# Optimization experiments

Measured on AMD Instinct MI355X. Metric: run time of the kernel, lower is better.

Reference implementation:

```python
import jax, jax.numpy as jnp
import numpy as np

N = 20000   # nodes
E = 320000  # edges
T = 12      # sequence_length
H = 64      # hidden_dim
CIN = 16    # input_dim_per_step
L = 3       # num_st_layers
BN_EPS = 1e-5


def setup_inputs() -> dict:
    key = jax.random.key(0)
    ks = jax.random.split(key, 30)
    s = 0.05
    rn = lambda k, shp: jax.random.normal(k, shp, jnp.float32) * s
    inp = {
        "x": jax.random.normal(ks[0], (N, T * CIN), jnp.float32),
        "edge_index": jax.random.randint(ks[1], (2, E), 0, N, jnp.int32),
        # embedding
        "We": rn(ks[2], (CIN, H)), "be": rn(ks[3], (H,)),
        # stacked per-layer params for the 3 ST layers
        "gcn_W": rn(ks[4], (L, H, H)), "gcn_b": rn(ks[5], (L, H)),
        "conv_w": rn(ks[6], (L, H, H, 3)), "conv_b": rn(ks[7], (L, H)),
        "bn_g": jnp.ones((L, H), jnp.float32), "bn_b": rn(ks[8], (L, H)),
        "bn_m": rn(ks[9], (L, H)),
        "bn_v": jax.random.uniform(ks[10], (L, H), jnp.float32, 0.5, 1.5),
        # temporal attention MLP (H -> H//2 -> 1)
        "ta_w1": rn(ks[11], (H, H // 2)), "ta_b1": rn(ks[12], (H // 2,)),
        "ta_w2": rn(ks[13], (H // 2, 1)), "ta_b2": rn(ks[14], (1,)),
        # feature attention MLP (T -> T//2 -> 1)
        "fa_w1": rn(ks[15], (T, T // 2)), "fa_b1": rn(ks[16], (T // 2,)),
        "fa_w2": rn(ks[17], (T // 2, 1)), "fa_b2": rn(ks[18], (1,)),
        # output MLP (H -> H//2 -> 1)
        "ow1": rn(ks[19], (H, H // 2)), "ob1": rn(ks[20], (H // 2,)),
        "ow2": rn(ks[21], (H // 2, 1)), "ob2": rn(ks[22], (1,)),
    }
    return inp


def reference(x, edge_index, We, be, gcn_W, gcn_b, conv_w, conv_b,
              bn_g, bn_b, bn_m, bn_v, ta_w1, ta_b1, ta_w2, ta_b2,
              fa_w1, fa_b1, fa_w2, fa_b2, ow1, ob1, ow2, ob2):
    n = x.shape[0]
    # --- GCN normalization with self-loops (PyG gcn_norm) ---
    loops = jnp.arange(n, dtype=edge_index.dtype)
    src = jnp.concatenate([edge_index[0], loops])
    dst = jnp.concatenate([edge_index[1], loops])
    deg = jax.ops.segment_sum(jnp.ones_like(src, jnp.float32), dst, num_segments=n)
    dinv = 1.0 / jnp.sqrt(deg)  # deg >= 1 thanks to self-loops
    coef = dinv[src] * dinv[dst]  # [E+N]

    # --- per-timestep embedding (vectorized over t) ---
    xr = x.reshape(n, T, CIN)
    emb = jax.nn.relu(jnp.einsum('ntc,ch->nth', xr, We) + be)  # [N,T,H]
    x_st = emb.reshape(n, T * H)

    # --- ST layers (replicating original row-major .view layout mixing) ---
    for i in range(L):
        xi = x_st.reshape(n, H, T)  # [N,C,T]
        # GCNConv per timestep, batched over t: linear then normalized aggregate
        h = jnp.einsum('nct,cd->ndt', xi, gcn_W[i])          # [N,H,T]
        msg = coef[:, None, None] * h[src]                   # [E+N,H,T]
        agg = jax.ops.segment_sum(msg, dst, num_segments=n) + gcn_b[i][None, :, None]
        # temporal conv (kernel 3, pad 1) over T
        tmp = jax.lax.conv_general_dilated(
            agg, conv_w[i], (1,), [(1, 1)],
            dimension_numbers=('NCH', 'OIH', 'NCH')) + conv_b[i][None, :, None]
        # BatchNorm1d (eval mode: running stats)
        normed = (tmp - bn_m[i][None, :, None]) / jnp.sqrt(bn_v[i][None, :, None] + BN_EPS)
        normed = normed * bn_g[i][None, :, None] + bn_b[i][None, :, None]
        # residual is Identity (in_channels == out_channels)
        x_st = jax.nn.relu(normed + xi).reshape(n, H * T)

    # --- dual attention pooling ---
    xa = x_st.reshape(n, T, H)
    tw = (jnp.einsum('ntm,mk->ntk', jax.nn.relu(jnp.einsum('nth,hm->ntm', xa, ta_w1) + ta_b1), ta_w2) + ta_b2)[..., 0]
    tw = jax.nn.softmax(tw, axis=1)                          # [N,T]
    xt = (xa * tw[..., None]).transpose(0, 2, 1)             # [N,H,T]
    fw = (jnp.einsum('nhm,mk->nhk', jax.nn.relu(jnp.einsum('nht,tm->nhm', xt, fa_w1) + fa_b1), fa_w2) + fa_b2)[..., 0]
    fw = jax.nn.softmax(fw, axis=1)                          # [N,H]
    x_final = jnp.sum(xt * fw[..., None], axis=2)            # [N,H]

    # --- output MLP (dropout is identity in eval) ---
    out = jax.nn.relu(x_final @ ow1 + ob1) @ ow2 + ob2       # [N,1]
    return out
```

## Files before the change

kernel.cpp:

```cpp
#include <hip/hip_runtime.h>
#include <cstddef>
#include <cstdint>

#define T_ 12
#define H_ 64
#define CIN_ 16
#define F_ 768
#define BN_EPS 1e-5f
#define ECAP 80
#define RPITCH 88
#define SLOTS 64

typedef float v2f __attribute__((ext_vector_type(2)));
typedef short s8v __attribute__((ext_vector_type(8)));
typedef float f4v __attribute__((ext_vector_type(4)));

__device__ __forceinline__ unsigned short f2bf(float f) {
    unsigned u = __float_as_uint(f);
    unsigned r = (u + 0x7FFFu + ((u >> 16) & 1u)) >> 16;
    return (unsigned short)r;
}
__device__ __forceinline__ float bf2f(unsigned short h) {
    return __uint_as_float(((unsigned)h) << 16);
}
__device__ __forceinline__ v2f bf2x2(unsigned u) {
    v2f r;
    r.x = __uint_as_float(u << 16);
    r.y = __uint_as_float(u & 0xFFFF0000u);
    return r;
}
__device__ __forceinline__ v2f pkfma(v2f a, v2f b, v2f c) {
    return __builtin_elementwise_fma(a, b, c);
}


__global__ void k_init(int* __restrict__ cursor, int n) {
    int i = blockIdx.x * 256 + threadIdx.x;
    if (i < n) cursor[i] = 0;
}


__global__ __launch_bounds__(256) void k_fused(
        const float* __restrict__ gcn_W, const float* __restrict__ gcn_b,
        const float* __restrict__ conv_w,
        float* __restrict__ wkp, float* __restrict__ bkp,
        const int* __restrict__ srcv, const int* __restrict__ dstv,
        int* __restrict__ cursor, int* __restrict__ csr_src, int e,
        const float* __restrict__ x, const float* __restrict__ We,
        const float* __restrict__ be, unsigned short* __restrict__ xbf, int nT,
        int nbE) {
    __shared__ float sW[CIN_ * H_];
    __shared__ float sb[H_];
    int b = blockIdx.x;
    int tid = threadIdx.x;

    if (b < 36) {
        int l = b / 12, k = (b / 4) % 3, cq = b & 3;
        const float* Wg = gcn_W + (size_t)l * 4096;
        const float* cw = conv_w + (size_t)l * 12288;
#pragma unroll
        for (int j = 0; j < 4; j++) {
            int idx = j * 256 + tid;
            int c = cq * 16 + (idx >> 6);
            int o = idx & 63;
            float acc = 0.f;
            for (int d = 0; d < 64; d++)
                acc += Wg[c * 64 + d] * cw[(size_t)(o * 64 + d) * 3 + k];
            wkp[(((size_t)l * 3 + k) * 64 + c) * 64 + o] = acc;
        }
        if (cq == 0 && tid < 64) {
            int o = tid;
            const float* gb = gcn_b + (size_t)l * 64;
            float acc = 0.f;
            for (int d = 0; d < 64; d++)
                acc += gb[d] * cw[(size_t)(o * 64 + d) * 3 + k];
            bkp[((size_t)l * 3 + k) * 64 + o] = acc;
        }
        return;
    }
    if (b < 36 + nbE) {
        int i = (b - 36) * 256 + tid;
        if (i < e) {
            int d = dstv[i], s = srcv[i];
            int pos = atomicAdd(&cursor[d], 1);
            if (pos < SLOTS) csr_src[d * SLOTS + pos] = s;
        }
        return;
    }
    for (int i = tid; i < CIN_ * H_; i += 256) sW[i] = We[i];
    if (tid < H_) sb[tid] = be[tid];
    __syncthreads();
    int h4  = tid & 15;
    int ntl = tid >> 4;
    int nt  = (b - 36 - nbE) * 16 + ntl;
    if (nt >= nT) return;
    const float4* xp = (const float4*)(x + (size_t)nt * CIN_);
    float4 xv4[4];
    xv4[0] = xp[0]; xv4[1] = xp[1]; xv4[2] = xp[2]; xv4[3] = xp[3];
    const float* xs = (const float*)xv4;
    float acc[4];
#pragma unroll
    for (int j = 0; j < 4; j++) acc[j] = sb[h4 * 4 + j];
#pragma unroll
    for (int c = 0; c < CIN_; c++) {
        float4 w = *(const float4*)&sW[c * H_ + h4 * 4];
        float xc = xs[c];
        acc[0] += xc * w.x; acc[1] += xc * w.y;
        acc[2] += xc * w.z; acc[3] += xc * w.w;
    }
    ushort4 h;
    h.x = f2bf(fmaxf(acc[0], 0.f)); h.y = f2bf(fmaxf(acc[1], 0.f));
    h.z = f2bf(fmaxf(acc[2], 0.f)); h.w = f2bf(fmaxf(acc[3], 0.f));
    *(ushort4*)&xbf[(size_t)nt * H_ + h4 * 4] = h;
}


__global__ __launch_bounds__(256) void k_post(
        const float* __restrict__ wkp, unsigned short* __restrict__ wkA,
        const int* __restrict__ cursor, const int* __restrict__ csr_src,
        float* __restrict__ csr_coef, float* __restrict__ dinv, int n) {
    int b = blockIdx.x;
    int tid = threadIdx.x;
    if (b < 18) {
        int wave = tid >> 6, lane = tid & 63;
        int job = b * 4 + wave;
        int l = job / 24, rem = job % 24;
        int mt = rem / 6, ks = rem % 6;
        int o = mt * 16 + (lane & 15);
        int kbase = ks * 32 + (lane >> 4) * 8;
#pragma unroll
        for (int j = 0; j < 8; j++) {
            int k = kbase + j;
            int kk = k >> 6, c = k & 63;
            float v = wkp[(((size_t)l * 3 + kk) * 64 + c) * 64 + o];
            wkA[((((size_t)l * 24) + mt * 6 + ks) * 64 + lane) * 8 + j] = f2bf(v);
        }
        return;
    }
    int i = (b - 18) * 256 + tid;
    int node = i >> 6, slot = i & 63;
    if (node >= n) return;
    int deg = cursor[node];
    float dn = rsqrtf((float)(deg + 1));
    if (slot == 0) dinv[node] = dn;
    if (slot < min(deg, SLOTS)) {
        int s = csr_src[node * SLOTS + slot];
        csr_coef[node * SLOTS + slot] = rsqrtf((float)(cursor[s] + 1)) * dn;
    }
}


#define BPK(aL, aH, c2, u) { \
    aL = pkfma(bf2x2((u).x), c2, aL); \
    aH = pkfma(bf2x2((u).y), c2, aH); }

#define LAYER_GATHER_CONV()                                                    \
    int tid = threadIdx.x;                                                     \
    int n0 = blockIdx.x * 8;                                                   \
    int wave = tid >> 6, lane = tid & 63;                                      \
    int wbase = wave * (ECAP * 2);                                             \
    for (int i = tid; i < 8 * 2 * RPITCH; i += 256) {                          \
        int s = i / (2 * RPITCH);                                              \
        int r = i - s * (2 * RPITCH);                                          \
        int row = (r < RPITCH) ? 0 : 13;                                       \
        int c = (r < RPITCH) ? r : r - RPITCH;                                 \
        sxb[s * 14 * RPITCH + row * RPITCH + c] = 0;                           \
    }                                                                          \
    int begs[2], cnts[2], stgs[2], epos[2];                                    \
    {                                                                          \
        int pos = 0;                                                           \
        for (int si = 0; si < 2; si++) {                                       \
            int nn = n0 + wave * 2 + si; if (nn >= n) nn = n - 1;              \
            int beg = nn * SLOTS;                                              \
            int cnt = min(degv[nn], SLOTS);                                    \
            int stg = min(cnt, ECAP - pos);                                    \
            for (int i = lane; i < stg; i += 64) {                             \
                se[wbase + (pos + i) * 2]     = csr_src[beg + i];              \
                se[wbase + (pos + i) * 2 + 1] = __float_as_int(csr_coef[beg + i]); \
            }                                                                  \
            begs[si] = beg; cnts[si] = cnt; stgs[si] = stg; epos[si] = pos;    \
            pos += stg;                                                        \
        }                                                                      \
    }                                                                          \
    {                                                                          \
        int i0 = 3 * lane;                                                     \
        for (int si = 0; si < 2; si++) {                                       \
            int s = wave * 2 + si;                                             \
            int nn = n0 + s; if (nn >= n) nn = n - 1;                          \
            float dn = dinv[nn];                                               \
            float cs = dn * dn;                                                \
            v2f cs2 = {cs, cs};                                                \
            const uint2* xp = (const uint2*)(xin + (size_t)nn * F_);           \
            uint2 u0 = xp[i0], u1 = xp[i0 + 1], u2 = xp[i0 + 2];               \
            v2f a0 = bf2x2(u0.x) * cs2, a1 = bf2x2(u0.y) * cs2;                \
            v2f a2 = bf2x2(u1.x) * cs2, a3 = bf2x2(u1.y) * cs2;                \
            v2f a4 = bf2x2(u2.x) * cs2, a5 = bf2x2(u2.y) * cs2;                \
            int cnt = stgs[si];                                                \
            int base = wbase + epos[si] * 2;                                   \
            int e = 0;                                                         \
            for (; e + 3 < cnt; e += 4) {                                      \
                int2 p0 = *(const int2*)&se[base + e * 2];                     \
                int2 p1 = *(const int2*)&se[base + e * 2 + 2];                 \
                int2 p2 = *(const int2*)&se[base + e * 2 + 4];                 \
                int2 p3 = *(const int2*)&se[base + e * 2 + 6];                 \
                const uint2* pA = (const uint2*)(xin + (size_t)p0.x * F_);     \
                const uint2* pB = (const uint2*)(xin + (size_t)p1.x * F_);     \
                const uint2* pC = (const uint2*)(xin + (size_t)p2.x * F_);     \
                const uint2* pD = (const uint2*)(xin + (size_t)p3.x * F_);     \
                uint2 uA0 = pA[i0], uA1 = pA[i0 + 1], uA2 = pA[i0 + 2];        \
                uint2 uB0 = pB[i0], uB1 = pB[i0 + 1], uB2 = pB[i0 + 2];        \
                uint2 uC0 = pC[i0], uC1 = pC[i0 + 1], uC2 = pC[i0 + 2];        \
                uint2 uD0 = pD[i0], uD1 = pD[i0 + 1], uD2 = pD[i0 + 2];        \
                float cA = __int_as_float(p0.y), cB = __int_as_float(p1.y);    \
                float cC = __int_as_float(p2.y), cD = __int_as_float(p3.y);    \
                v2f cA2 = {cA, cA}, cB2 = {cB, cB};                            \
                v2f cC2 = {cC, cC}, cD2 = {cD, cD};                            \
                BPK(a0, a1, cA2, uA0) BPK(a2, a3, cA2, uA1) BPK(a4, a5, cA2, uA2) \
                BPK(a0, a1, cB2, uB0) BPK(a2, a3, cB2, uB1) BPK(a4, a5, cB2, uB2) \
                BPK(a0, a1, cC2, uC0) BPK(a2, a3, cC2, uC1) BPK(a4, a5, cC2, uC2) \
                BPK(a0, a1, cD2, uD0) BPK(a2, a3, cD2, uD1) BPK(a4, a5, cD2, uD2) \
            }                                                                  \
            for (; e < cnt; e++) {                                             \
                int2 p0 = *(const int2*)&se[base + e * 2];                     \
                const uint2* pA = (const uint2*)(xin + (size_t)p0.x * F_);     \
                uint2 uA0 = pA[i0], uA1 = pA[i0 + 1], uA2 = pA[i0 + 2];        \
                float cA = __int_as_float(p0.y);                               \
                v2f cA2 = {cA, cA};                                            \
                BPK(a0, a1, cA2, uA0) BPK(a2, a3, cA2, uA1) BPK(a4, a5, cA2, uA2) \
            }                                                                  \
            for (int g = begs[si] + stgs[si]; g < begs[si] + cnts[si]; g++) {  \
                int srcI = csr_src[g];                                         \
                float cf = csr_coef[g];                                        \
                const uint2* pA = (const uint2*)(xin + (size_t)srcI * F_);     \
                uint2 uA0 = pA[i0], uA1 = pA[i0 + 1], uA2 = pA[i0 + 2];        \
                v2f cf2 = {cf, cf};                                            \
                BPK(a0, a1, cf2, uA0) BPK(a2, a3, cf2, uA1) BPK(a4, a5, cf2, uA2) \
            }                                                                  \
            unsigned short* wp = &sxb[s * 14 * RPITCH + RPITCH + lane];        \
            float vals[12] = {a0.x, a0.y, a1.x, a1.y, a2.x, a2.y,              \
                              a3.x, a3.y, a4.x, a4.y, a5.x, a5.y};             \
            for (int t = 0; t < 12; t++) wp[t * RPITCH] = f2bf(vals[t]);       \
        }                                                                      \
    }                                                                          \
    __syncthreads();                                                           \
    int mt = wave;                                                             \
    int q = lane >> 4;                                                         \
    int l15 = lane & 15;                                                       \
    s8v afr[6];                                                                \
    const s8v* Ap = (const s8v*)wkA;                                           \
    for (int ks = 0; ks < 6; ks++) afr[ks] = Ap[(mt * 6 + ks) * 64 + lane];    \
    int obase = mt * 16 + q * 4;                                               \
    float scl[4], shf[4], ball[4], bk0a[4], bk2a[4];                           \
    for (int r = 0; r < 4; r++) {                                              \
        int o = obase + r;                                                     \
        float sc = bng[o] * rsqrtf(bnv[o] + BN_EPS);                           \
        scl[r] = sc;                                                           \
        shf[r] = bnb[o] - bnm[o] * sc;                                         \
        float b0 = bkp[o], b1 = bkp[64 + o], b2 = bkp[128 + o];                \
        ball[r] = cb[o] + b0 + b1 + b2;                                        \
        bk0a[r] = b0; bk2a[r] = b2;                                            \
    }                                                                          \
    f4v accv[6];                                                               \
    for (int nt = 0; nt < 6; nt++) {                                           \
        int nidx = nt * 16 + l15;                                              \
        int s = nidx / 12, t = nidx - 12 * s;                                  \
        const s8v* bp = (const s8v*)&sxb[s * 14 * RPITCH + t * RPITCH + q * 8];\
        f4v acc = {0.f, 0.f, 0.f, 0.f};                                        \
        acc = __builtin_amdgcn_mfma_f32_16x16x32_bf16(afr[0], bp[0],  acc, 0, 0, 0); \
        acc = __builtin_amdgcn_mfma_f32_16x16x32_bf16(afr[1], bp[4],  acc, 0, 0, 0); \
        acc = __builtin_amdgcn_mfma_f32_16x16x32_bf16(afr[2], bp[11], acc, 0, 0, 0); \
        acc = __builtin_amdgcn_mfma_f32_16x16x32_bf16(afr[3], bp[15], acc, 0, 0, 0); \
        acc = __builtin_amdgcn_mfma_f32_16x16x32_bf16(afr[4], bp[22], acc, 0, 0, 0); \
        acc = __builtin_amdgcn_mfma_f32_16x16x32_bf16(afr[5], bp[26], acc, 0, 0, 0); \
        accv[nt] = acc;                                                        \
    }                                                                          \
    __syncthreads();                                                           \
    for (int nt = 0; nt < 6; nt++) {                                           \
        int nidx = nt * 16 + l15;                                              \
        int s = nidx / 12, t = nidx - 12 * s;                                  \
        unsigned short* dp = &sxb[s * F_ + t];                                 \
        for (int r = 0; r < 4; r++) {                                          \
            float bias = ball[r];                                              \
            if (t == 0)  bias -= bk0a[r];                                      \
            if (t == 11) bias -= bk2a[r];                                      \
            float v = (accv[nt][r] + bias) * scl[r] + shf[r];                  \
            dp[(obase + r) * 12] = f2bf(v);                                    \
        }                                                                      \
    }                                                                          \
    __syncthreads();


__global__ __launch_bounds__(256, 7) void k_layer(
        const unsigned short* __restrict__ xin,
        unsigned short* __restrict__ xout,
        const int* __restrict__ degv, const int* __restrict__ csr_src,
        const float* __restrict__ csr_coef, const float* __restrict__ dinv,
        const unsigned short* __restrict__ wkA,
        const float* __restrict__ bkp, const float* __restrict__ cb,
        const float* __restrict__ bng, const float* __restrict__ bnb,
        const float* __restrict__ bnm, const float* __restrict__ bnv,
        int n) {
    __shared__ __align__(16) unsigned short sxb[8 * 14 * RPITCH];
    __shared__ int se[4 * ECAP * 2];
    LAYER_GATHER_CONV()

#pragma unroll
    for (int cidx = 0; cidx < 3; cidx++) {
        int c = cidx * 256 + tid;
        int s = c / 96, off = c - s * 96;
        int nn = n0 + s;
        if (nn >= n) continue;
        uint4 dv = *(const uint4*)&sxb[s * F_ + off * 8];
        uint4 rv = ((const uint4*)(xin + (size_t)nn * F_))[off];
        uint4 ov;
        unsigned* dvp = (unsigned*)&dv;
        unsigned* rvp = (unsigned*)&rv;
        unsigned* ovp = (unsigned*)&ov;
#pragma unroll
        for (int w = 0; w < 4; w++) {
            v2f d2 = bf2x2(dvp[w]);
            v2f r2 = bf2x2(rvp[w]);
            float lo = fmaxf(d2.x + r2.x, 0.f);
            float hi = fmaxf(d2.y + r2.y, 0.f);
            ovp[w] = (unsigned)f2bf(lo) | ((unsigned)f2bf(hi) << 16);
        }
        *(uint4*)(xout + (size_t)nn * F_ + off * 8) = ov;
    }
}


__global__ __launch_bounds__(256, 6) void k_layer_attn(
        const unsigned short* __restrict__ xin,
        const int* __restrict__ degv, const int* __restrict__ csr_src,
        const float* __restrict__ csr_coef, const float* __restrict__ dinv,
        const unsigned short* __restrict__ wkA,
        const float* __restrict__ bkp, const float* __restrict__ cb,
        const float* __restrict__ bng, const float* __restrict__ bnb,
        const float* __restrict__ bnm, const float* __restrict__ bnv,
        const float* __restrict__ taw1, const float* __restrict__ tab1,
        const float* __restrict__ taw2, const float* __restrict__ tab2,
        const float* __restrict__ faw1, const float* __restrict__ fab1,
        const float* __restrict__ faw2, const float* __restrict__ fab2,
        const float* __restrict__ ow1, const float* __restrict__ ob1,
        const float* __restrict__ ow2, const float* __restrict__ ob2,
        float* __restrict__ out, int n) {
    __shared__ __align__(16) unsigned short sxb[8 * 14 * RPITCH];
    __shared__ int se[4 * ECAP * 2];
    LAYER_GATHER_CONV()

#pragma unroll
    for (int cidx = 0; cidx < 3; cidx++) {
        int c = cidx * 256 + tid;
        int s = c / 96, off = c - s * 96;
        int nn = n0 + s; if (nn >= n) nn = n - 1;
        uint4 dv = *(const uint4*)&sxb[s * F_ + off * 8];
        uint4 rv = ((const uint4*)(xin + (size_t)nn * F_))[off];
        unsigned* dvp = (unsigned*)&dv;
        unsigned* rvp = (unsigned*)&rv;
#pragma unroll
        for (int w = 0; w < 4; w++) {
            v2f d2 = bf2x2(dvp[w]);
            v2f r2 = bf2x2(rvp[w]);
            float lo = fmaxf(d2.x + r2.x, 0.f);
            float hi = fmaxf(d2.y + r2.y, 0.f);
            dvp[w] = (unsigned)f2bf(lo) | ((unsigned)f2bf(hi) << 16);
        }
        *(uint4*)&sxb[s * F_ + off * 8] = dv;
    }
    __syncthreads();

    float* s_tw = (float*)se;
    float* s_xf = (float*)se + 96;

    {
        int s2 = tid >> 5, m = tid & 31;
        float a[12];
        float bm = tab1[m];
#pragma unroll
        for (int t = 0; t < 12; t++) a[t] = bm;
        const unsigned short* xr = &sxb[s2 * F_];
        float tb2 = tab2[0];
        for (int hh = 0; hh < 64; hh++) {
            const uint2* xp2 = (const uint2*)&xr[hh * 12];
            uint2 w0 = xp2[0], w1 = xp2[1], w2 = xp2[2];
            v2f x0 = bf2x2(w0.x), x1 = bf2x2(w0.y), x2 = bf2x2(w1.x);
            v2f x3 = bf2x2(w1.y), x4 = bf2x2(w2.x), x5 = bf2x2(w2.y);
            float xv[12] = {x0.x, x0.y, x1.x, x1.y, x2.x, x2.y,
                            x3.x, x3.y, x4.x, x4.y, x5.x, x5.y};
            float wv = taw1[hh * 32 + m];
#pragma unroll
            for (int t = 0; t < 12; t++) a[t] += wv * xv[t];
        }
        float w2v = taw2[m];
#pragma unroll
        for (int t = 0; t < 12; t++) {
            float p = fmaxf(a[t], 0.f) * w2v;
            p += __shfl_xor(p, 1); p += __shfl_xor(p, 2);
            p += __shfl_xor(p, 4); p += __shfl_xor(p, 8);
            p += __shfl_xor(p, 16);
            if (m == 0) s_tw[s2 * 12 + t] = p + tb2;
        }
    }
    __syncthreads();

    {
        float fb2 = fab2[0];
        for (int qi = 0; qi < 2; qi++) {
            int ss = wave * 2 + qi;
            float tw[12];
#pragma unroll
            for (int t = 0; t < 12; t++) tw[t] = s_tw[ss * 12 + t];
            float mx = tw[0];
#pragma unroll
            for (int t = 1; t < 12; t++) mx = fmaxf(mx, tw[t]);
            float sum = 0.f;
#pragma unroll
            for (int t = 0; t < 12; t++) { tw[t] = __expf(tw[t] - mx); sum += tw[t]; }
            float inv = 1.f / sum;
            const uint2* xp2 = (const uint2*)&sxb[ss * F_ + lane * 12];
            uint2 w0 = xp2[0], w1 = xp2[1], w2 = xp2[2];
            v2f x0 = bf2x2(w0.x), x1 = bf2x2(w0.y), x2 = bf2x2(w1.x);
            v2f x3 = bf2x2(w1.y), x4 = bf2x2(w2.x), x5 = bf2x2(w2.y);
            float xv[12] = {x0.x, x0.y, x1.x, x1.y, x2.x, x2.y,
                            x3.x, x3.y, x4.x, x4.y, x5.x, x5.y};
            float xt[12];
#pragma unroll
            for (int t = 0; t < 12; t++) xt[t] = xv[t] * tw[t] * inv;
            float lf = fb2;
#pragma unroll
            for (int mm = 0; mm < 6; mm++) {
                float v = fab1[mm];
#pragma unroll
                for (int t = 0; t < 12; t++) v += xt[t] * faw1[t * 6 + mm];
                lf += fmaxf(v, 0.f) * faw2[mm];
            }
            float m2v = lf;
#pragma unroll
            for (int off = 32; off >= 1; off >>= 1)
                m2v = fmaxf(m2v, __shfl_xor(m2v, off));
            float ev = __expf(lf - m2v);
            float sev = ev;
#pragma unroll
            for (int off = 32; off >= 1; off >>= 1) sev += __shfl_xor(sev, off);
            float fwv = ev / sev;
            float xs = 0.f;
#pragma unroll
            for (int t = 0; t < 12; t++) xs += xt[t];
            s_xf[ss * 65 + lane] = fwv * xs;
        }
    }
    __syncthreads();

    {
        int s2 = tid >> 5, m = tid & 31;
        float v = ob1[m];
        const float* xfp = &s_xf[s2 * 65];
        for (int hh = 0; hh < 64; hh++) v += xfp[hh] * ow1[hh * 32 + m];
        float p = fmaxf(v, 0.f) * ow2[m];
        p += __shfl_xor(p, 1); p += __shfl_xor(p, 2);
        p += __shfl_xor(p, 4); p += __shfl_xor(p, 8);
        p += __shfl_xor(p, 16);
        if (m == 0 && n0 + s2 < n) out[n0 + s2] = p + ob2[0];
    }
}


extern "C" void kernel_launch(void* const* d_in, const int* in_sizes, int n_in,
                              void* d_out, int out_size, void* d_ws, size_t ws_size,
                              hipStream_t stream) {
    const float* x      = (const float*)d_in[0];
    const int*   ei     = (const int*)d_in[1];
    const float* We     = (const float*)d_in[2];
    const float* be     = (const float*)d_in[3];
    const float* gcn_W  = (const float*)d_in[4];
    const float* gcn_b  = (const float*)d_in[5];
    const float* conv_w = (const float*)d_in[6];
    const float* conv_b = (const float*)d_in[7];
    const float* bn_g   = (const float*)d_in[8];
    const float* bn_b   = (const float*)d_in[9];
    const float* bn_m   = (const float*)d_in[10];
    const float* bn_v   = (const float*)d_in[11];
    const float* ta_w1  = (const float*)d_in[12];
    const float* ta_b1  = (const float*)d_in[13];
    const float* ta_w2  = (const float*)d_in[14];
    const float* ta_b2  = (const float*)d_in[15];
    const float* fa_w1  = (const float*)d_in[16];
    const float* fa_b1  = (const float*)d_in[17];
    const float* fa_w2  = (const float*)d_in[18];
    const float* fa_b2  = (const float*)d_in[19];
    const float* ow1    = (const float*)d_in[20];
    const float* ob1    = (const float*)d_in[21];
    const float* ow2    = (const float*)d_in[22];
    const float* ob2    = (const float*)d_in[23];

    int n = in_sizes[0] / (T_ * CIN_);
    int e = in_sizes[1] / 2;
    const int* srcv = ei;
    const int* dstv = ei + e;

    char* p = (char*)d_ws;
    auto take = [&](size_t bytes) -> void* {
        void* r = (void*)p;
        p += (bytes + 255) & ~(size_t)255;
        return r;
    };
    int*   cursor    = (int*)take((size_t)n * 4);
    float* dinv      = (float*)take((size_t)n * 4);
    int*   csr_src   = (int*)take((size_t)n * SLOTS * 4);
    float* csr_coef  = (float*)take((size_t)n * SLOTS * 4);
    float* wkp       = (float*)take((size_t)3 * 3 * 64 * 64 * 4);
    float* bkp       = (float*)take((size_t)3 * 3 * 64 * 4);
    unsigned short* wkA = (unsigned short*)take((size_t)3 * 24 * 64 * 8 * 2);
    unsigned short* xabf = (unsigned short*)take((size_t)n * F_ * 2);
    unsigned short* xbbf = (unsigned short*)take((size_t)n * F_ * 2);

    int nb_n = (n + 255) / 256;
    int nb_e = (e + 255) / 256;
    int nb8  = (n + 7) / 8;
    int nT   = n * T_;
    int nbM  = (nT + 15) / 16;

    k_init<<<nb_n, 256, 0, stream>>>(cursor, n);
    k_fused<<<36 + nb_e + nbM, 256, 0, stream>>>(
        gcn_W, gcn_b, conv_w, wkp, bkp,
        srcv, dstv, cursor, csr_src, e,
        x, We, be, xabf, nT, nb_e);
    k_post<<<18 + (n * SLOTS + 255) / 256, 256, 0, stream>>>(
        wkp, wkA, cursor, csr_src, csr_coef, dinv, n);

    k_layer<<<nb8, 256, 0, stream>>>(xabf, xbbf, cursor, csr_src, csr_coef,
                                     dinv, wkA, bkp, conv_b,
                                     bn_g, bn_b, bn_m, bn_v, n);
    k_layer<<<nb8, 256, 0, stream>>>(xbbf, xabf, cursor, csr_src, csr_coef,
                                     dinv, wkA + (size_t)1 * 24 * 64 * 8,
                                     bkp + (size_t)1 * 3 * 64,
                                     conv_b + (size_t)1 * H_,
                                     bn_g + (size_t)1 * H_, bn_b + (size_t)1 * H_,
                                     bn_m + (size_t)1 * H_, bn_v + (size_t)1 * H_,
                                     n);
    k_layer_attn<<<nb8, 256, 0, stream>>>(xabf, cursor, csr_src, csr_coef,
                                          dinv, wkA + (size_t)2 * 24 * 64 * 8,
                                          bkp + (size_t)2 * 3 * 64,
                                          conv_b + (size_t)2 * H_,
                                          bn_g + (size_t)2 * H_, bn_b + (size_t)2 * H_,
                                          bn_m + (size_t)2 * H_, bn_v + (size_t)2 * H_,
                                          ta_w1, ta_b1, ta_w2, ta_b2,
                                          fa_w1, fa_b1, fa_w2, fa_b2,
                                          ow1, ob1, ow2, ob2, (float*)d_out, n);
}
```

Before: 415.4 us.

## Software-pipeline edge gathers with double buffers and scalarize uniform row indices

The neighbor-gather loop is restructured into a two-stage software pipeline: the next group of four edge rows is loaded into a second register buffer while the current group is accumulated, so memory latency overlaps the packed FMAs. Row indices that are wave-uniform go through readfirstlane so address computation can use scalar registers. Occupancy is lowered from 7 to 6 waves per SIMD to make room for the extra registers, and the temporal-attention matvec is rewritten with packed FMAs. The gain in latency hiding is traded against fewer resident waves.

Measured after the change: 572.5 us. 37.8% more time.

```diff
diff --git a/kernel.cpp b/kernel.cpp
--- a/kernel.cpp
+++ b/kernel.cpp
@@ -153,6 +153,36 @@
 #define BPK(aL, aH, c2, u) { \
     aL = pkfma(bf2x2((u).x), c2, aL); \
     aH = pkfma(bf2x2((u).y), c2, aH); }
+
+#define GLD_E(EA, EB_) { \
+    EA[0] = *(const int2*)&se[base + (EB_) * 2]; \
+    EA[1] = *(const int2*)&se[base + (EB_) * 2 + 2]; \
+    EA[2] = *(const int2*)&se[base + (EB_) * 2 + 4]; \
+    EA[3] = *(const int2*)&se[base + (EB_) * 2 + 6]; }
+
+#define GLD_F(EA, BUF) { \
+    int sR0_ = __builtin_amdgcn_readfirstlane(EA[0].x); \
+    int sR1_ = __builtin_amdgcn_readfirstlane(EA[1].x); \
+    int sR2_ = __builtin_amdgcn_readfirstlane(EA[2].x); \
+    int sR3_ = __builtin_amdgcn_readfirstlane(EA[3].x); \
+    const uint2* pA_ = (const uint2*)(xin + (size_t)sR0_ * F_); \
+    const uint2* pB_ = (const uint2*)(xin + (size_t)sR1_ * F_); \
+    const uint2* pC_ = (const uint2*)(xin + (size_t)sR2_ * F_); \
+    const uint2* pD_ = (const uint2*)(xin + (size_t)sR3_ * F_); \
+    BUF[0] = pA_[i0]; BUF[1]  = pA_[i0 + 1]; BUF[2]  = pA_[i0 + 2]; \
+    BUF[3] = pB_[i0]; BUF[4]  = pB_[i0 + 1]; BUF[5]  = pB_[i0 + 2]; \
+    BUF[6] = pC_[i0]; BUF[7]  = pC_[i0 + 1]; BUF[8]  = pC_[i0 + 2]; \
+    BUF[9] = pD_[i0]; BUF[10] = pD_[i0 + 1]; BUF[11] = pD_[i0 + 2]; }
+
+#define GCONS(EA, BUF) { \
+    float cA = __int_as_float(EA[0].y), cB = __int_as_float(EA[1].y); \
+    float cC = __int_as_float(EA[2].y), cD = __int_as_float(EA[3].y); \
+    v2f cA2 = {cA, cA}, cB2 = {cB, cB}; \
+    v2f cC2 = {cC, cC}, cD2 = {cD, cD}; \
+    BPK(a0, a1, cA2, BUF[0]) BPK(a2, a3, cA2, BUF[1]) BPK(a4, a5, cA2, BUF[2]) \
+    BPK(a0, a1, cB2, BUF[3]) BPK(a2, a3, cB2, BUF[4]) BPK(a4, a5, cB2, BUF[5]) \
+    BPK(a0, a1, cC2, BUF[6]) BPK(a2, a3, cC2, BUF[7]) BPK(a4, a5, cC2, BUF[8]) \
+    BPK(a0, a1, cD2, BUF[9]) BPK(a2, a3, cD2, BUF[10]) BPK(a4, a5, cD2, BUF[11]) }
 
 #define LAYER_GATHER_CONV()                                                    \
     int tid = threadIdx.x;                                                     \
@@ -187,49 +217,49 @@
         for (int si = 0; si < 2; si++) {                                       \
             int s = wave * 2 + si;                                             \
             int nn = n0 + s; if (nn >= n) nn = n - 1;                          \
-            float dn = dinv[nn];                                               \
+            int nnU = __builtin_amdgcn_readfirstlane(nn);                      \
+            float dn = dinv[nnU];                                              \
             float cs = dn * dn;                                                \
             v2f cs2 = {cs, cs};                                                \
-            const uint2* xp = (const uint2*)(xin + (size_t)nn * F_);           \
+            const uint2* xp = (const uint2*)(xin + (size_t)nnU * F_);          \
             uint2 u0 = xp[i0], u1 = xp[i0 + 1], u2 = xp[i0 + 2];               \
             v2f a0 = bf2x2(u0.x) * cs2, a1 = bf2x2(u0.y) * cs2;                \
             v2f a2 = bf2x2(u1.x) * cs2, a3 = bf2x2(u1.y) * cs2;                \
             v2f a4 = bf2x2(u2.x) * cs2, a5 = bf2x2(u2.y) * cs2;                \
             int cnt = stgs[si];                                                \
             int base = wbase + epos[si] * 2;                                   \
-            int e = 0;                                                         \
-            for (; e + 3 < cnt; e += 4) {                                      \
-                int2 p0 = *(const int2*)&se[base + e * 2];                     \
-                int2 p1 = *(const int2*)&se[base + e * 2 + 2];                 \
-                int2 p2 = *(const int2*)&se[base + e * 2 + 4];                 \
-                int2 p3 = *(const int2*)&se[base + e * 2 + 6];                 \
-                const uint2* pA = (const uint2*)(xin + (size_t)p0.x * F_);     \
-                const uint2* pB = (const uint2*)(xin + (size_t)p1.x * F_);     \
-                const uint2* pC = (const uint2*)(xin + (size_t)p2.x * F_);     \
-                const uint2* pD = (const uint2*)(xin + (size_t)p3.x * F_);     \
-                uint2 uA0 = pA[i0], uA1 = pA[i0 + 1], uA2 = pA[i0 + 2];        \
-                uint2 uB0 = pB[i0], uB1 = pB[i0 + 1], uB2 = pB[i0 + 2];        \
-                uint2 uC0 = pC[i0], uC1 = pC[i0 + 1], uC2 = pC[i0 + 2];        \
-                uint2 uD0 = pD[i0], uD1 = pD[i0 + 1], uD2 = pD[i0 + 2];        \
-                float cA = __int_as_float(p0.y), cB = __int_as_float(p1.y);    \
-                float cC = __int_as_float(p2.y), cD = __int_as_float(p3.y);    \
-                v2f cA2 = {cA, cA}, cB2 = {cB, cB};                            \
-                v2f cC2 = {cC, cC}, cD2 = {cD, cD};                            \
-                BPK(a0, a1, cA2, uA0) BPK(a2, a3, cA2, uA1) BPK(a4, a5, cA2, uA2) \
-                BPK(a0, a1, cB2, uB0) BPK(a2, a3, cB2, uB1) BPK(a4, a5, cB2, uB2) \
-                BPK(a0, a1, cC2, uC0) BPK(a2, a3, cC2, uC1) BPK(a4, a5, cC2, uC2) \
-                BPK(a0, a1, cD2, uD0) BPK(a2, a3, cD2, uD1) BPK(a4, a5, cD2, uD2) \
+            int nb4 = cnt >> 2;                                                \
+            int e = nb4 << 2;                                                  \
+            if (nb4 > 0) {                                                     \
+                int2 eA[4], eB[4];                                             \
+                uint2 bA[12], bB[12];                                          \
+                GLD_E(eA, 0) GLD_F(eA, bA)                                     \
+                int e4 = 1;                                                    \
+                for (; e4 + 1 < nb4; e4 += 2) {                                \
+                    GLD_E(eB, e4 * 4) GLD_F(eB, bB)                            \
+                    GCONS(eA, bA)                                              \
+                    GLD_E(eA, e4 * 4 + 4) GLD_F(eA, bA)                        \
+                    GCONS(eB, bB)                                              \
+                }                                                              \
+                if (e4 < nb4) {                                                \
+                    GLD_E(eB, e4 * 4) GLD_F(eB, bB)                            \
+                    GCONS(eA, bA)                                              \
+                    GCONS(eB, bB)                                              \
+                } else {                                                       \
+                    GCONS(eA, bA)                                              \
+                }                                                              \
             }                                                                  \
             for (; e < cnt; e++) {                                             \
                 int2 p0 = *(const int2*)&se[base + e * 2];                     \
-                const uint2* pA = (const uint2*)(xin + (size_t)p0.x * F_);     \
+                int sE_ = __builtin_amdgcn_readfirstlane(p0.x);                \
+                const uint2* pA = (const uint2*)(xin + (size_t)sE_ * F_);      \
                 uint2 uA0 = pA[i0], uA1 = pA[i0 + 1], uA2 = pA[i0 + 2];        \
                 float cA = __int_as_float(p0.y);                               \
                 v2f cA2 = {cA, cA};                                            \
                 BPK(a0, a1, cA2, uA0) BPK(a2, a3, cA2, uA1) BPK(a4, a5, cA2, uA2) \
             }                                                                  \
             for (int g = begs[si] + stgs[si]; g < begs[si] + cnts[si]; g++) {  \
-                int srcI = csr_src[g];                                         \
+                int srcI = __builtin_amdgcn_readfirstlane(csr_src[g]);         \
                 float cf = csr_coef[g];                                        \
                 const uint2* pA = (const uint2*)(xin + (size_t)srcI * F_);     \
                 uint2 uA0 = pA[i0], uA1 = pA[i0 + 1], uA2 = pA[i0 + 2];        \
@@ -290,7 +320,7 @@
     __syncthreads();
 
 
-__global__ __launch_bounds__(256, 7) void k_layer(
+__global__ __launch_bounds__(256, 6) void k_layer(
         const unsigned short* __restrict__ xin,
         unsigned short* __restrict__ xout,
         const int* __restrict__ degv, const int* __restrict__ csr_src,
@@ -374,27 +404,29 @@
 
     {
         int s2 = tid >> 5, m = tid & 31;
-        float a[12];
         float bm = tab1[m];
-#pragma unroll
-        for (int t = 0; t < 12; t++) a[t] = bm;
+        v2f aa0 = {bm, bm}, aa1 = aa0, aa2 = aa0;
+        v2f aa3 = aa0, aa4 = aa0, aa5 = aa0;
         const unsigned short* xr = &sxb[s2 * F_];
         float tb2 = tab2[0];
         for (int hh = 0; hh < 64; hh++) {
             const uint2* xp2 = (const uint2*)&xr[hh * 12];
             uint2 w0 = xp2[0], w1 = xp2[1], w2 = xp2[2];
-            v2f x0 = bf2x2(w0.x), x1 = bf2x2(w0.y), x2 = bf2x2(w1.x);
-            v2f x3 = bf2x2(w1.y), x4 = bf2x2(w2.x), x5 = bf2x2(w2.y);
-            float xv[12] = {x0.x, x0.y, x1.x, x1.y, x2.x, x2.y,
-                            x3.x, x3.y, x4.x, x4.y, x5.x, x5.y};
             float wv = taw1[hh * 32 + m];
-#pragma unroll
-            for (int t = 0; t < 12; t++) a[t] += wv * xv[t];
+            v2f wv2 = {wv, wv};
+            aa0 = pkfma(bf2x2(w0.x), wv2, aa0);
+            aa1 = pkfma(bf2x2(w0.y), wv2, aa1);
+            aa2 = pkfma(bf2x2(w1.x), wv2, aa2);
+            aa3 = pkfma(bf2x2(w1.y), wv2, aa3);
+            aa4 = pkfma(bf2x2(w2.x), wv2, aa4);
+            aa5 = pkfma(bf2x2(w2.y), wv2, aa5);
         }
         float w2v = taw2[m];
+        float av[12] = {aa0.x, aa0.y, aa1.x, aa1.y, aa2.x, aa2.y,
+                        aa3.x, aa3.y, aa4.x, aa4.y, aa5.x, aa5.y};
 #pragma unroll
         for (int t = 0; t < 12; t++) {
-            float p = fmaxf(a[t], 0.f) * w2v;
+            float p = fmaxf(av[t], 0.f) * w2v;
             p += __shfl_xor(p, 1); p += __shfl_xor(p, 2);
             p += __shfl_xor(p, 4); p += __shfl_xor(p, 8);
             p += __shfl_xor(p, 16);
```
